# Performance work log

Measured on AMD Instinct MI355X. Metric: run time of the kernel, lower is better.

## Reference

```python
import jax, jax.numpy as jnp
import numpy as np

EPS = 1e-7  # K.epsilon()


def setup_inputs() -> dict:
    key = jax.random.key(0)
    k1, k2, k3 = jax.random.split(key, 3)
    B, H, W, Cin, Cout, KH, KW = 8, 128, 128, 256, 256, 3, 3
    x = jax.random.normal(k1, (B, H, W, Cin), dtype=jnp.float32)
    style = jax.random.normal(k2, (B, Cin), dtype=jnp.float32)
    # he_uniform-ish scale for the kernel
    fan_in = KH * KW * Cin
    limit = np.sqrt(6.0 / fan_in)
    kernel = jax.random.uniform(k3, (KH, KW, Cin, Cout), dtype=jnp.float32,
                                minval=-limit, maxval=limit)
    return {"x": x, "style": style, "kernel": kernel}


def reference(x, style, kernel):
    # Demodulation factor: rsqrt(sum_{kh,kw,cin} (kernel * style)^2 + eps), shape (B, Cout).
    # Equivalent to the original's broadcast-then-reduce, computed without
    # materializing the (B,kh,kw,Cin,Cout) modulated weight tensor.
    k2 = jnp.sum(jnp.square(kernel), axis=(0, 1))          # (Cin, Cout)
    ssq = jnp.einsum('io,bi->bo', k2, jnp.square(style))   # (B, Cout)
    demod = jax.lax.rsqrt(ssq + EPS)                       # (B, Cout)

    # Modulate input per-sample, then shared-weight conv (same padding, stride 1).
    xm = x * style[:, None, None, :]                       # (B,H,W,Cin)
    y = jax.lax.conv_general_dilated(
        xm, kernel,
        window_strides=(1, 1), padding='SAME',
        dimension_numbers=('NHWC', 'HWIO', 'NHWC'))
    return y * demod[:, None, None, :]
```

## Files before the change

### kernel.cpp

```cpp
#include <hip/hip_runtime.h>
#include <hip/hip_bf16.h>
#include <stdint.h>

typedef short short8 __attribute__((ext_vector_type(8)));
typedef float f32x4 __attribute__((ext_vector_type(4)));

#define KKTOT 2304
#define PXS   40

__device__ __forceinline__ short f2bf(float f) {
    __hip_bfloat16 h = __float2bfloat16(f);
    return __builtin_bit_cast(short, h);
}

__global__ void prep_demod(const float* __restrict__ style,
                           const float* __restrict__ kern,
                           float* __restrict__ demod)
{
    const int b = blockIdx.x, co = threadIdx.x;
    float acc = 0.f;
    for (int ci = 0; ci < 256; ++ci) {
        float s = style[b * 256 + ci];
        float k2 = 0.f;
#pragma unroll
        for (int p = 0; p < 9; ++p) {
            float w = kern[(p * 256 + ci) * 256 + co];
            k2 += w * w;
        }
        acc += s * s * k2;
    }
    demod[b * 256 + co] = 1.0f / sqrtf(acc + 1e-7f);
}

__global__ void prep_kt(const float* __restrict__ kern,
                        __hip_bfloat16* __restrict__ kT)
{
    __shared__ float tile[64][65];
    const int t   = threadIdx.x;
    const int k0  = blockIdx.x << 6;
    const int c0  = blockIdx.y << 6;
    const int col = t & 63;
    const int rb  = (t >> 6) << 4;
#pragma unroll
    for (int r = 0; r < 16; ++r) {
        int kl = rb + r;
        tile[kl][col] = kern[(size_t)(k0 + kl) * 256 + c0 + col];
    }
    __syncthreads();
#pragma unroll
    for (int r = 0; r < 16; ++r) {
        int co = rb + r;
        kT[(size_t)(c0 + co) * KKTOT + k0 + col] = __float2bfloat16(tile[col][co]);
    }
}

__global__ __launch_bounds__(256) void conv_mfma(
    const float* __restrict__ x,
    const __hip_bfloat16* __restrict__ kt,
    const float* __restrict__ style,
    const float* __restrict__ demod,
    float* __restrict__ out)
{
    __shared__ __align__(16) __hip_bfloat16 Xs[130 * PXS];
    __shared__ __align__(16) __hip_bfloat16 Bs[3 * 128 * PXS];
    __shared__ float Ss[256];
    __shared__ float Ds[128];

    const int t    = threadIdx.x;
    const int n0   = blockIdx.x << 7;
    const int bh   = blockIdx.y;
    const int b    = bh >> 7, h = bh & 127;
    const int wave = t >> 6, lane = t & 63;
    const int wr   = (wave >> 1) << 6;
    const int wc   = (wave & 1) << 6;
    const int l15  = lane & 15, lk = lane >> 4;
    const int mA   = t >> 2;
    const int koff = (t & 3) << 3;

    if (t < 128) {
        ((float2*)Ss)[t] = ((const float2*)(style + b * 256))[t];
        Ds[t] = demod[b * 256 + n0 + t];
    }
    if (t < 32) {
        Xs[t]             = __float2bfloat16(0.f);
        Xs[129 * PXS + t] = __float2bfloat16(0.f);
    }

    f32x4 acc[4][4] = {};

    for (int sl = 0; sl < 24; ++sl) {
        const int h2 = h + (sl >> 3) - 1;
        if ((unsigned)h2 >= 128u) continue;
        const int ci0     = (sl & 7) << 5;
        const int posbase = (sl >> 3) * 3;

        __syncthreads();

        const size_t rowbase = (size_t)(b * 128 + h2) * 128;
        const float* ga = x + (rowbase + mA)      * 256 + ci0 + koff;
        const float* gb = x + (rowbase + mA + 64) * 256 + ci0 + koff;
        float4 xa0 = *(const float4*)ga,       xa1 = *(const float4*)(ga + 4);
        float4 xb0 = *(const float4*)gb,       xb1 = *(const float4*)(gb + 4);
        float4 s0  = *(const float4*)&Ss[ci0 + koff];
        float4 s1  = *(const float4*)&Ss[ci0 + koff + 4];
        short8 ma, mb;
#pragma unroll
        for (int jj = 0; jj < 4; ++jj) {
            ma[jj]     = f2bf((&xa0.x)[jj] * (&s0.x)[jj]);
            ma[jj + 4] = f2bf((&xa1.x)[jj] * (&s1.x)[jj]);
            mb[jj]     = f2bf((&xb0.x)[jj] * (&s0.x)[jj]);
            mb[jj + 4] = f2bf((&xb1.x)[jj] * (&s1.x)[jj]);
        }
        *(short8*)&Xs[(mA + 1)  * PXS + koff] = ma;
        *(short8*)&Xs[(mA + 65) * PXS + koff] = mb;

        const __hip_bfloat16* gw =
            kt + (size_t)(n0 + mA) * KKTOT + posbase * 256 + ci0 + koff;
#pragma unroll
        for (int tp = 0; tp < 3; ++tp) {
            short8 w0 = *(const short8*)(gw + tp * 256);
            short8 w1 = *(const short8*)(gw + tp * 256 + 64 * KKTOT);
            *(short8*)&Bs[tp * (128 * PXS) + mA * PXS + koff]        = w0;
            *(short8*)&Bs[tp * (128 * PXS) + (mA + 64) * PXS + koff] = w1;
        }
        __syncthreads();

#pragma unroll
        for (int tp = 0; tp < 3; ++tp) {
            short8 af[4], bfr[4];
#pragma unroll
            for (int i = 0; i < 4; ++i)
                af[i] = *(const short8*)&Xs[(wr + i * 16 + l15 + tp) * PXS + lk * 8];
#pragma unroll
            for (int j = 0; j < 4; ++j)
                bfr[j] = *(const short8*)&Bs[tp * (128 * PXS) + (wc + j * 16 + l15) * PXS + lk * 8];
#pragma unroll
            for (int i = 0; i < 4; ++i)
#pragma unroll
                for (int j = 0; j < 4; ++j)
                    acc[i][j] = __builtin_amdgcn_mfma_f32_16x16x32_bf16(
                        af[i], bfr[j], acc[i][j], 0, 0, 0);
        }
    }

    float dj[4];
#pragma unroll
    for (int j = 0; j < 4; ++j) dj[j] = Ds[wc + j * 16 + l15];
    const size_t obase = (size_t)(b * 128 + h) * 128 * 256 + n0;
#pragma unroll
    for (int i = 0; i < 4; ++i) {
#pragma unroll
        for (int j = 0; j < 4; ++j) {
            const int n = wc + j * 16 + l15;
#pragma unroll
            for (int r = 0; r < 4; ++r) {
                const int m = wr + i * 16 + lk * 4 + r;
                out[obase + (size_t)m * 256 + n] = acc[i][j][r] * dj[j];
            }
        }
    }
}

extern "C" void kernel_launch(void* const* d_in, const int* in_sizes, int n_in,
                              void* d_out, int out_size, void* d_ws, size_t ws_size,
                              hipStream_t stream)
{
    const float* x     = (const float*)d_in[0];
    const float* style = (const float*)d_in[1];
    const float* kern  = (const float*)d_in[2];
    float* out = (float*)d_out;

    char*  ws    = (char*)d_ws;
    float* demod = (float*)ws;
    __hip_bfloat16* kT = (__hip_bfloat16*)(ws + 8192);

    prep_demod<<<8, 256, 0, stream>>>(style, kern, demod);
    prep_kt   <<<dim3(36, 4), 256, 0, stream>>>(kern, kT);
    conv_mfma <<<dim3(2, 1024), 256, 0, stream>>>(x, kT, style, demod, out);
}
```

Measured before the change: 435.1 us.

## Parallelize demod prep via K2 kernel and swizzle conv blocks across XCDs

```diff
diff --git a/kernel.cpp b/kernel.cpp
--- a/kernel.cpp
+++ b/kernel.cpp
@@ -13,22 +13,31 @@
     return __builtin_bit_cast(short, h);
 }
 
+__global__ void prep_k2(const float* __restrict__ kern, float* __restrict__ K2)
+{
+    const int ci = blockIdx.x, co = threadIdx.x;
+    float acc = 0.f;
+#pragma unroll
+    for (int p = 0; p < 9; ++p) {
+        float w = kern[(p * 256 + ci) * 256 + co];
+        acc += w * w;
+    }
+    K2[ci * 256 + co] = acc;
+}
+
 __global__ void prep_demod(const float* __restrict__ style,
-                           const float* __restrict__ kern,
+                           const float* __restrict__ K2,
                            float* __restrict__ demod)
 {
     const int b = blockIdx.x, co = threadIdx.x;
+    __shared__ float s2[256];
+    float s = style[b * 256 + co];
+    s2[co] = s * s;
+    __syncthreads();
     float acc = 0.f;
-    for (int ci = 0; ci < 256; ++ci) {
-        float s = style[b * 256 + ci];
-        float k2 = 0.f;
-#pragma unroll
-        for (int p = 0; p < 9; ++p) {
-            float w = kern[(p * 256 + ci) * 256 + co];
-            k2 += w * w;
-        }
-        acc += s * s * k2;
-    }
+#pragma unroll 8
+    for (int ci = 0; ci < 256; ++ci)
+        acc += s2[ci] * K2[ci * 256 + co];
     demod[b * 256 + co] = 1.0f / sqrtf(acc + 1e-7f);
 }
 
@@ -67,8 +76,10 @@
     __shared__ float Ds[128];
 
     const int t    = threadIdx.x;
-    const int n0   = blockIdx.x << 7;
-    const int bh   = blockIdx.y;
+    const int bid  = blockIdx.x;
+    const int L    = ((bid & 7) << 8) | (bid >> 3);
+    const int n0   = (L & 1) << 7;
+    const int bh   = L >> 1;
     const int b    = bh >> 7, h = bh & 127;
     const int wave = t >> 6, lane = t & 63;
     const int wr   = (wave >> 1) << 6;
@@ -172,9 +183,11 @@
 
     char*  ws    = (char*)d_ws;
     float* demod = (float*)ws;
-    __hip_bfloat16* kT = (__hip_bfloat16*)(ws + 8192);
+    float* K2    = (float*)(ws + 8192);
+    __hip_bfloat16* kT = (__hip_bfloat16*)(ws + 270336);
 
-    prep_demod<<<8, 256, 0, stream>>>(style, kern, demod);
+    prep_k2   <<<256, 256, 0, stream>>>(kern, K2);
+    prep_demod<<<8,   256, 0, stream>>>(style, K2, demod);
     prep_kt   <<<dim3(36, 4), 256, 0, stream>>>(kern, kT);
-    conv_mfma <<<dim3(2, 1024), 256, 0, stream>>>(x, kT, style, demod, out);
+    conv_mfma <<<2048, 256, 0, stream>>>(x, kT, style, demod, out);
 }
```

New measurement: 361.9 us. 1.2x faster.
